# Optimization experiments

Measured on AMD Instinct MI355X. Metric: run time of the kernel, lower is better.

The kernel has to match this reference:

```python
import jax, jax.numpy as jnp
import numpy as np

N_EMBD = 1024
N_HEADS = 16
HEAD_SIZE = N_EMBD // N_HEADS
B, T = 1, 4096
LN_EPS = 1e-5


def setup_inputs() -> dict:
    key = jax.random.key(0)
    ks = jax.random.split(key, 12)
    s = lambda fan_in: 1.0 / np.sqrt(fan_in)
    return {
        "x": jax.random.normal(ks[0], (B, T, N_EMBD), dtype=jnp.float32),
        # per-head Q/K/V projections (no bias), stacked over heads: [H, C, hd]
        "Wq": jax.random.normal(ks[1], (N_HEADS, N_EMBD, HEAD_SIZE), dtype=jnp.float32) * s(N_EMBD),
        "Wk": jax.random.normal(ks[2], (N_HEADS, N_EMBD, HEAD_SIZE), dtype=jnp.float32) * s(N_EMBD),
        "Wv": jax.random.normal(ks[3], (N_HEADS, N_EMBD, HEAD_SIZE), dtype=jnp.float32) * s(N_EMBD),
        # output projection (with bias)
        "Wp": jax.random.normal(ks[4], (N_EMBD, N_EMBD), dtype=jnp.float32) * s(N_EMBD),
        "bp": jnp.zeros((N_EMBD,), dtype=jnp.float32),
        # FFN: Linear(C, 4C) -> ReLU -> Linear(4C, C)
        "W1": jax.random.normal(ks[5], (N_EMBD, 4 * N_EMBD), dtype=jnp.float32) * s(N_EMBD),
        "b1": jnp.zeros((4 * N_EMBD,), dtype=jnp.float32),
        "W2": jax.random.normal(ks[6], (4 * N_EMBD, N_EMBD), dtype=jnp.float32) * s(4 * N_EMBD),
        "b2": jnp.zeros((N_EMBD,), dtype=jnp.float32),
        # LayerNorms
        "g1": jnp.ones((N_EMBD,), dtype=jnp.float32),
        "be1": jnp.zeros((N_EMBD,), dtype=jnp.float32),
        "g2": jnp.ones((N_EMBD,), dtype=jnp.float32),
        "be2": jnp.zeros((N_EMBD,), dtype=jnp.float32),
    }


def _layernorm(x, gamma, beta):
    mu = jnp.mean(x, axis=-1, keepdims=True)
    var = jnp.mean(jnp.square(x - mu), axis=-1, keepdims=True)
    return (x - mu) * jax.lax.rsqrt(var + LN_EPS) * gamma + beta


def _block(x, Wq, Wk, Wv, Wp, bp, W1, b1, W2, b2, g1, be1, g2, be2):
    Bn, Tn, C = x.shape
    h = _layernorm(x, g1, be1)
    # per-head projections: [B, H, T, hd]
    q = jnp.einsum("btc,hcd->bhtd", h, Wq)
    k = jnp.einsum("btc,hcd->bhtd", h, Wk)
    v = jnp.einsum("btc,hcd->bhtd", h, Wv)
    # NOTE: original scales by C**-0.5 where C = n_embd (not head_size)
    scores = jnp.einsum("bhtd,bhsd->bhts", q, k) * (C ** -0.5)
    causal = jnp.tril(jnp.ones((Tn, Tn), dtype=bool))
    scores = jnp.where(causal, scores, -jnp.inf)
    w = jax.nn.softmax(scores, axis=-1)
    attn = jnp.einsum("bhts,bhsd->bhtd", w, v)
    # concat heads: [B, T, H*hd] = [B, T, C]
    attn = attn.transpose(0, 2, 1, 3).reshape(Bn, Tn, C)
    x = x + attn @ Wp + bp
    h2 = _layernorm(x, g2, be2)
    ff = jax.nn.relu(h2 @ W1 + b1) @ W2 + b2
    return x + ff


def reference(x, Wq, Wk, Wv, Wp, bp, W1, b1, W2, b2, g1, be1, g2, be2):
    return _block(x, Wq, Wk, Wv, Wp, bp, W1, b1, W2, b2, g1, be1, g2, be2)
```

## Files before the change

kernel.cpp:

```cpp
#include <hip/hip_runtime.h>
#include <cstdint>

typedef __attribute__((ext_vector_type(8))) short bf16x8;
typedef __attribute__((ext_vector_type(4))) float f32x4;
typedef __attribute__((ext_vector_type(16))) float f32x16;
typedef __attribute__((ext_vector_type(4))) unsigned int u32x4;

__device__ __forceinline__ short f2b(float f) {
  unsigned u = __builtin_bit_cast(unsigned, f);
  unsigned r = (u + 0x7fffu + ((u >> 16) & 1u)) >> 16;
  return (short)(unsigned short)r;
}
__device__ __forceinline__ float b2f(short s) {
  unsigned u = ((unsigned)(unsigned short)s) << 16;
  return __builtin_bit_cast(float, u);
}

__device__ __forceinline__ void gload16(void* lds_dst, const void* gsrc) {
  __builtin_amdgcn_global_load_lds(
      (const __attribute__((address_space(1))) void*)gsrc,
      (__attribute__((address_space(3))) void*)lds_dst, 16, 0, 0);
}

__device__ __forceinline__ unsigned cvtpk(float a, float b) {
  unsigned r;
  asm("v_cvt_pk_bf16_f32 %0, %1, %2" : "=v"(r) : "v"(a), "v"(b));
  return r;
}
__device__ __forceinline__ unsigned shflx32(unsigned v) {
  return (unsigned)__shfl_xor((int)v, 32);
}
__device__ __forceinline__ float exp2x(float x) {
  float r;
  asm("v_exp_f32 %0, %1" : "=v"(r) : "v"(x));
  return r;
}

__device__ __forceinline__ void plswap(unsigned &a, unsigned &b) {
#if __has_builtin(__builtin_amdgcn_permlane32_swap)
  auto r = __builtin_amdgcn_permlane32_swap((int)a, (int)b, false, false);
  a = (unsigned)r[0];
  b = (unsigned)r[1];
#else
  const bool lo = ((threadIdx.x & 63) < 32);
  unsigned ax = shflx32(a), bx = shflx32(b);
  unsigned na = lo ? a : bx;
  unsigned nb = lo ? ax : b;
  a = na; b = nb;
#endif
}

__global__ __launch_bounds__(256)
void prep_all(const float* __restrict__ Wq, const float* __restrict__ Wk,
              const float* __restrict__ Wv, const float* __restrict__ Wp,
              const float* __restrict__ W1, const float* __restrict__ W2,
              const float* __restrict__ x, const float* __restrict__ g1,
              const float* __restrict__ be1,
              short* __restrict__ WqkvT, short* __restrict__ WpT,
              short* __restrict__ W1T, short* __restrict__ W2T,
              short* __restrict__ hbuf)
{
  const int id = blockIdx.x;
  if (id < 12288) {
    __shared__ float tl[32][33];
    const int tx = threadIdx.x & 31;
    const int ty = threadIdx.x >> 5;
    if (id < 3072) {
      const int which = id >> 10;
      const int rem = id & 1023;
      const int head = rem >> 6;
      const int tile = rem & 63;
      const int tc = tile >> 1, td = tile & 1;
      const float* src = (which == 0 ? Wq : which == 1 ? Wk : Wv) + (long)head * 65536;
#pragma unroll
      for (int i2 = 0; i2 < 4; ++i2) {
        int i = ty + i2 * 8;
        tl[i][tx] = src[(long)(tc * 32 + i) * 64 + td * 32 + tx];
      }
      __syncthreads();
      const long base = (long)which * 1024 + head * 64 + td * 32;
#pragma unroll
      for (int i2 = 0; i2 < 4; ++i2) {
        int i = ty + i2 * 8;
        WqkvT[(base + i) * 1024 + tc * 32 + tx] = f2b(tl[tx][i]);
      }
    } else {
      const float* src;
      short* dst;
      int rows, cols, bx, by;
      if (id < 4096) {
        src = Wp; dst = WpT; rows = 1024; cols = 1024;
        const int k = id - 3072; bx = k & 31; by = k >> 5;
      } else if (id < 8192) {
        src = W1; dst = W1T; rows = 1024; cols = 4096;
        const int k = id - 4096; bx = k & 127; by = k >> 7;
      } else {
        src = W2; dst = W2T; rows = 4096; cols = 1024;
        const int k = id - 8192; bx = k & 31; by = k >> 5;
      }
#pragma unroll
      for (int i2 = 0; i2 < 4; ++i2) {
        int i = ty + i2 * 8;
        tl[i][tx] = src[(long)(by * 32 + i) * cols + bx * 32 + tx];
      }
      __syncthreads();
#pragma unroll
      for (int i2 = 0; i2 < 4; ++i2) {
        int i = ty + i2 * 8;
        dst[(long)(bx * 32 + i) * rows + by * 32 + tx] = f2b(tl[tx][i]);
      }
    }
  } else {
    const int row = id - 12288;
    const int t = threadIdx.x;
    const float4 v = ((const float4*)(x + (long)row * 1024))[t];
    float s = v.x + v.y + v.z + v.w;
    float ss = v.x * v.x + v.y * v.y + v.z * v.z + v.w * v.w;
#pragma unroll
    for (int off = 1; off < 64; off <<= 1) {
      s += __shfl_xor(s, off);
      ss += __shfl_xor(ss, off);
    }
    __shared__ float red[8];
    const int wave = t >> 6, lane = t & 63;
    if (lane == 0) { red[wave] = s; red[4 + wave] = ss; }
    __syncthreads();
    s = red[0] + red[1] + red[2] + red[3];
    ss = red[4] + red[5] + red[6] + red[7];
    const float mu = s * (1.f / 1024.f);
    const float rstd = rsqrtf(ss * (1.f / 1024.f) - mu * mu + 1e-5f);
    const float4 gv = ((const float4*)g1)[t];
    const float4 bv = ((const float4*)be1)[t];
    short4 ov;
    ov.x = f2b((v.x - mu) * rstd * gv.x + bv.x);
    ov.y = f2b((v.y - mu) * rstd * gv.y + bv.y);
    ov.z = f2b((v.z - mu) * rstd * gv.z + bv.z);
    ov.w = f2b((v.w - mu) * rstd * gv.w + bv.w);
    *(short4*)(hbuf + (long)row * 1024 + t * 4) = ov;
  }
}

__global__ void vtrans(const short* __restrict__ qkv, short* __restrict__ Vt)
{
  __shared__ short tl[32][33];
  const int t0 = blockIdx.x * 32;
  const int c0 = blockIdx.y * 32;
  const int head = c0 >> 6, d0 = c0 & 63;
  const int tx = threadIdx.x;
#pragma unroll
  for (int i2 = 0; i2 < 4; ++i2) {
    int i = threadIdx.y + i2 * 8;
    tl[i][tx] = qkv[(long)(t0 + i) * 3072 + 2048 + c0 + tx];
  }
  __syncthreads();
#pragma unroll
  for (int i2 = 0; i2 < 4; ++i2) {
    int i = threadIdx.y + i2 * 8;
    Vt[(long)head * 262144 + (long)(d0 + i) * 4096 + t0 + tx] = tl[tx][i];
  }
}

__global__ __launch_bounds__(256)
void layernorm_bf16(const float* __restrict__ x, const float* __restrict__ g,
                    const float* __restrict__ be, short* __restrict__ outp)
{
  const int row = blockIdx.x;
  const int t = threadIdx.x;
  const float4 v = ((const float4*)(x + (long)row * 1024))[t];
  float s = v.x + v.y + v.z + v.w;
  float ss = v.x * v.x + v.y * v.y + v.z * v.z + v.w * v.w;
#pragma unroll
  for (int off = 1; off < 64; off <<= 1) {
    s += __shfl_xor(s, off);
    ss += __shfl_xor(ss, off);
  }
  __shared__ float red[8];
  const int wave = t >> 6, lane = t & 63;
  if (lane == 0) { red[wave] = s; red[4 + wave] = ss; }
  __syncthreads();
  s = red[0] + red[1] + red[2] + red[3];
  ss = red[4] + red[5] + red[6] + red[7];
  const float mu = s * (1.f / 1024.f);
  const float rstd = rsqrtf(ss * (1.f / 1024.f) - mu * mu + 1e-5f);
  const float4 gv = ((const float4*)g)[t];
  const float4 bv = ((const float4*)be)[t];
  short4 ov;
  ov.x = f2b((v.x - mu) * rstd * gv.x + bv.x);
  ov.y = f2b((v.y - mu) * rstd * gv.y + bv.y);
  ov.z = f2b((v.z - mu) * rstd * gv.z + bv.z);
  ov.w = f2b((v.w - mu) * rstd * gv.w + bv.w);
  *(short4*)(outp + (long)row * 1024 + t * 4) = ov;
}

template<int EPI>
__global__ __launch_bounds__(512, 2)
void gemm128(const short* __restrict__ A, const short* __restrict__ Bt,
             int N, int K, int NT,
             short* __restrict__ Cb, float* __restrict__ Cf,
             const float* __restrict__ bias, const float* __restrict__ resid)
{
  __shared__ __align__(16) short As[2 * 8192];
  __shared__ __align__(16) short Bs[2 * 8192];
  const int tid = threadIdx.x;
  const int lane = tid & 63;
  const int wave = tid >> 6;
  const int wm = wave >> 2;
  const int wn = wave & 3;
  const int l15 = lane & 15, lg = lane >> 4;

  const int nwg = gridDim.x * gridDim.y;
  const int lin = blockIdx.y * gridDim.x + blockIdx.x;
  const int swz = (lin & 7) * (nwg >> 3) + (lin >> 3);
  const long m0 = (long)(swz / gridDim.x) * 128;
  const long n0 = (long)(swz % gridDim.x) * 128;

  const int rloc = lane >> 3;
  const int csrc = (lane & 7) ^ rloc;
  const short* Ag = A + (m0 + wave * 8 + rloc) * K + csrc * 8;
  const short* Bg = Bt + (n0 + wave * 8 + rloc) * K + csrc * 8;
  const int wbase = wave * 512;

  f32x4 acc[4][2] = {};

#define STAGE128(buf, kt)                                                     \
  do {                                                                        \
    gload16(As + (buf) * 8192 + wbase, Ag + (kt));                            \
    gload16(As + (buf) * 8192 + 4096 + wbase, Ag + (long)64 * K + (kt));      \
    gload16(Bs + (buf) * 8192 + wbase, Bg + (kt));                            \
    gload16(Bs + (buf) * 8192 + 4096 + wbase, Bg + (long)64 * K + (kt));      \
  } while (0)

  STAGE128(0, 0);
  STAGE128(1, 64);
  asm volatile("s_waitcnt vmcnt(4)" ::: "memory");
  __builtin_amdgcn_sched_barrier(0);
  __builtin_amdgcn_s_barrier();
  __builtin_amdgcn_sched_barrier(0);

  const int cA = l15 & 7;
  for (int t = 0; t < NT; ++t) {
    const char* Ab = (const char*)(As + (t & 1) * 8192);
    const char* Bb = (const char*)(Bs + (t & 1) * 8192);
#pragma unroll
    for (int kk = 0; kk < 2; ++kk) {
      bf16x8 af[4], bk[2];
#pragma unroll
      for (int mi = 0; mi < 4; ++mi)
        af[mi] = *(const bf16x8*)(Ab + (wm * 64 + mi * 16 + l15) * 128 + 16 * ((kk * 4 + lg) ^ cA));
#pragma unroll
      for (int ni = 0; ni < 2; ++ni)
        bk[ni] = *(const bf16x8*)(Bb + (wn * 32 + ni * 16 + l15) * 128 + 16 * ((kk * 4 + lg) ^ cA));
      __builtin_amdgcn_s_setprio(1);
#pragma unroll
      for (int mi = 0; mi < 4; ++mi)
#pragma unroll
        for (int ni = 0; ni < 2; ++ni)
          acc[mi][ni] = __builtin_amdgcn_mfma_f32_16x16x32_bf16(af[mi], bk[ni], acc[mi][ni], 0, 0, 0);
      __builtin_amdgcn_s_setprio(0);
    }
    if (t == NT - 1) break;
    __builtin_amdgcn_s_barrier();
    __builtin_amdgcn_sched_barrier(0);
    if (t + 2 < NT) {
      STAGE128(t & 1, (long)(t + 2) * 64);
      asm volatile("s_waitcnt vmcnt(4)" ::: "memory");
    } else {
      asm volatile("s_waitcnt vmcnt(0)" ::: "memory");
    }
    __builtin_amdgcn_sched_barrier(0);
    __builtin_amdgcn_s_barrier();
    __builtin_amdgcn_sched_barrier(0);
  }
#undef STAGE128

#pragma unroll
  for (int mi = 0; mi < 4; ++mi) {
#pragma unroll
    for (int ni = 0; ni < 2; ++ni) {
      const long col = n0 + wn * 32 + ni * 16 + l15;
#pragma unroll
      for (int r = 0; r < 4; ++r) {
        const long row = m0 + wm * 64 + mi * 16 + lg * 4 + r;
        const long idx = row * N + col;
        float v = acc[mi][ni][r];
        if (EPI == 0) {
          Cb[idx] = f2b(v);
        } else {
          Cf[idx] = v + bias[col] + resid[idx];
        }
      }
    }
  }
}

__device__ __forceinline__ void stage256(short* AsB, short* BsB,
                                         const short* Ag, const short* Bg,
                                         long kt, int K, int ldsoff)
{
#pragma unroll
  for (int p = 0; p < 4; ++p)
    gload16(AsB + p * 4096 + ldsoff, Ag + (long)p * 64 * K + kt);
#pragma unroll
  for (int p = 0; p < 4; ++p)
    gload16(BsB + p * 4096 + ldsoff, Bg + (long)p * 64 * K + kt);
}

template<int EPI>
__global__ __launch_bounds__(512, 2)
void gemm256(const short* __restrict__ A, const short* __restrict__ Bt,
             int N, int K, int NT,
             short* __restrict__ Cb, const float* __restrict__ bias)
{
  __shared__ __align__(16) short As[2 * 16384];
  __shared__ __align__(16) short Bs[2 * 16384];
  const int tid = threadIdx.x;
  const int lane = tid & 63;
  const int wave = tid >> 6;
  const int wm = wave >> 2;
  const int wn = wave & 3;
  const int l15 = lane & 15, lg = lane >> 4;

  const int nwg = gridDim.x * gridDim.y;
  const int lin = blockIdx.y * gridDim.x + blockIdx.x;
  const int swz = (lin & 7) * (nwg >> 3) + (lin >> 3);
  const long m0 = (long)(swz / gridDim.x) * 256;
  const long n0 = (long)(swz % gridDim.x) * 256;

  const int trow = tid >> 3;
  const int csrc = (tid & 7) ^ (trow & 7);
  const short* Ag = A + (m0 + trow) * K + csrc * 8;
  const short* Bg = Bt + (n0 + trow) * K + csrc * 8;
  const int ldsoff = wave * 512;

  f32x4 acc[8][4] = {};

  stage256(As, Bs, Ag, Bg, 0, K, ldsoff);
  asm volatile("s_waitcnt vmcnt(0)" ::: "memory");
  __builtin_amdgcn_sched_barrier(0);
  __builtin_amdgcn_s_barrier();
  __builtin_amdgcn_sched_barrier(0);

  const int cA = l15 & 7;
  for (int t = 0; t < NT; ++t) {
    const char* Ab = (const char*)(As + (t & 1) * 16384);
    const char* Bb = (const char*)(Bs + (t & 1) * 16384);
    short* Asn = As + ((t + 1) & 1) * 16384;
    short* Bsn = Bs + ((t + 1) & 1) * 16384;
    const bool more = (t + 1 < NT);
    const long ktn = (long)(t + 1) * 64;
    bf16x8 bk[4];
#pragma unroll
    for (int ph = 0; ph < 4; ++ph) {
      const int kk = ph >> 1;
      const int mh = (ph & 1) * 4;
      bf16x8 af[4];
#pragma unroll
      for (int mi = 0; mi < 4; ++mi)
        af[mi] = *(const bf16x8*)(Ab + (wm * 128 + (mh + mi) * 16 + l15) * 128 + 16 * ((kk * 4 + lg) ^ cA));
      if ((ph & 1) == 0) {
#pragma unroll
        for (int ni = 0; ni < 4; ++ni)
          bk[ni] = *(const bf16x8*)(Bb + (wn * 64 + ni * 16 + l15) * 128 + 16 * ((kk * 4 + lg) ^ cA));
      }
      if (more && ph == 0) {
#pragma unroll
        for (int p = 0; p < 4; ++p)
          gload16(Asn + p * 4096 + ldsoff, Ag + (long)p * 64 * K + ktn);
      }
      if (more && ph == 1) {
#pragma unroll
        for (int p = 0; p < 4; ++p)
          gload16(Bsn + p * 4096 + ldsoff, Bg + (long)p * 64 * K + ktn);
      }
      __builtin_amdgcn_s_barrier();
      asm volatile("s_waitcnt lgkmcnt(0)" ::: "memory");
      __builtin_amdgcn_sched_barrier(0);
      __builtin_amdgcn_s_setprio(1);
#pragma unroll
      for (int mi = 0; mi < 4; ++mi)
#pragma unroll
        for (int ni = 0; ni < 4; ++ni)
          acc[mh + mi][ni] = __builtin_amdgcn_mfma_f32_16x16x32_bf16(af[mi], bk[ni], acc[mh + mi][ni], 0, 0, 0);
      __builtin_amdgcn_s_setprio(0);
      if (ph == 3 && more) {
        asm volatile("s_waitcnt vmcnt(0)" ::: "memory");
        __builtin_amdgcn_sched_barrier(0);
      }
      __builtin_amdgcn_s_barrier();
      __builtin_amdgcn_sched_barrier(0);
    }
  }

#pragma unroll
  for (int mi = 0; mi < 8; ++mi) {
#pragma unroll
    for (int ni = 0; ni < 4; ++ni) {
      const long col = n0 + wn * 64 + ni * 16 + l15;
      const float bb = (EPI == 2) ? bias[col] : 0.f;
#pragma unroll
      for (int r = 0; r < 4; ++r) {
        const long row = m0 + wm * 128 + mi * 16 + lg * 4 + r;
        float v = acc[mi][ni][r];
        if (EPI == 2) { v += bb; v = v > 0.f ? v : 0.f; }
        Cb[row * N + col] = f2b(v);
      }
    }
  }
}

__device__ __forceinline__ void stage_k32(short* lds, const short* gRowBase)
{
  const int lane = threadIdx.x & 63;
  const int rloc = lane >> 3;
  const int cs = (lane & 7) ^ rloc;
#pragma unroll
  for (int p = 0; p < 4; ++p)
    gload16(lds + p * 512, gRowBase + (long)(p * 8 + rloc) * 3072 + cs * 8);
}
__device__ __forceinline__ void stage_v32(short* lds, const short* vHeadBase, int t0)
{
  const int lane = threadIdx.x & 63;
  const int rloc = lane >> 3;
  const int cs = (lane & 7) ^ rloc;
#pragma unroll
  for (int p = 0; p < 4; ++p) {
    const int row = p * 8 + rloc;
    const int d = row + ((cs & 4) << 3);
    gload16(lds + p * 512, vHeadBase + (long)d * 4096 + t0 + (cs & 3) * 8);
  }
}

__global__ __launch_bounds__(256)
void attn_fwd6(const short* __restrict__ qkv, const short* __restrict__ Vt,
               short* __restrict__ outp)
{
  __shared__ __align__(16) short POOL[4 * 4096];
  __shared__ float lAll[64];
  short* const OB = POOL;

  const int tid = threadIdx.x;
  const int lane = tid & 63;
  const int wave = tid >> 6;
  const int wq = wave & 1;
  const int ks = wave >> 1;
  const int l31 = lane & 31;
  const int h = lane >> 5;
  const int rs = l31 & 7;

  const int id = blockIdx.x;
  const int head = ((id & 7) << 1) | (id >> 8);
  const int bx = (id >> 3) & 31;

  const short* Qg = qkv + head * 64;
  const short* Kg = qkv + 1024 + head * 64;
  const short* Vg = Vt + (long)head * 262144;

  short* Kw = POOL + wave * 4096;

  bf16x8 onesf;
#pragma unroll
  for (int j = 0; j < 8; ++j) onesf[j] = (short)0x3F80;

  for (int ph = 0; ph < 2; ++ph) {
    const int qsuper = ph ? (63 - bx) : bx;
    const int q0 = qsuper * 64 + wq * 32;
    const int q = q0 + l31;
    const int nt = qsuper + 1;

    bf16x8 qf[4];
#pragma unroll
    for (int d = 0; d < 4; ++d) {
      bf16x8 tq = *(const bf16x8*)(Qg + (long)q * 3072 + d * 16 + h * 8);
#pragma unroll
      for (int j = 0; j < 8; ++j) tq[j] = f2b(b2f(tq[j]) * (0.03125f * 1.44269504f));
      qf[d] = tq;
    }

    f32x16 o0 = {}, o1 = {}, lacc = {};

    stage_k32(Kw, Kg + (long)(ks * 32) * 3072);
    stage_v32(Kw + 2048, Vg, ks * 32);

    for (int t = 0; t < nt; ++t) {
      asm volatile("s_waitcnt vmcnt(0)" ::: "memory");
      __builtin_amdgcn_sched_barrier(0);
      const char* Kb = (const char*)Kw;
      const char* Vb = Kb + 4096;
      const bf16x8 kf0 = *(const bf16x8*)(Kb + l31 * 128 + 16 * ((0 + h) ^ rs));
      const bf16x8 kf1 = *(const bf16x8*)(Kb + l31 * 128 + 16 * ((2 + h) ^ rs));
      const bf16x8 kf2 = *(const bf16x8*)(Kb + l31 * 128 + 16 * ((4 + h) ^ rs));
      const bf16x8 kf3 = *(const bf16x8*)(Kb + l31 * 128 + 16 * ((6 + h) ^ rs));
      const bf16x8 vf00 = *(const bf16x8*)(Vb + l31 * 128 + 16 * ((0 + h) ^ rs));
      const bf16x8 vf01 = *(const bf16x8*)(Vb + l31 * 128 + 16 * ((2 + h) ^ rs));
      const bf16x8 vf10 = *(const bf16x8*)(Vb + l31 * 128 + 16 * ((4 + h) ^ rs));
      const bf16x8 vf11 = *(const bf16x8*)(Vb + l31 * 128 + 16 * ((6 + h) ^ rs));
      asm volatile("s_waitcnt lgkmcnt(0)" ::: "memory");
      __builtin_amdgcn_sched_barrier(0);
      if (t + 1 < nt) {
        stage_k32(Kw, Kg + (long)((t + 1) * 64 + ks * 32) * 3072);
        stage_v32(Kw + 2048, Vg, (t + 1) * 64 + ks * 32);
      }
      f32x16 s = {};
      __builtin_amdgcn_s_setprio(1);
      s = __builtin_amdgcn_mfma_f32_32x32x16_bf16(kf0, qf[0], s, 0, 0, 0);
      s = __builtin_amdgcn_mfma_f32_32x32x16_bf16(kf1, qf[1], s, 0, 0, 0);
      s = __builtin_amdgcn_mfma_f32_32x32x16_bf16(kf2, qf[2], s, 0, 0, 0);
      s = __builtin_amdgcn_mfma_f32_32x32x16_bf16(kf3, qf[3], s, 0, 0, 0);
      __builtin_amdgcn_s_setprio(0);
      if (t == qsuper) {
        const int kb0 = t * 64 + ks * 32 + 4 * h;
#pragma unroll
        for (int r = 0; r < 16; ++r) {
          const int k0 = kb0 + (r & 3) + 8 * (r >> 2);
          if (k0 > q) s[r] = -INFINITY;
        }
      }
#pragma unroll
      for (int r = 0; r < 16; ++r) s[r] = exp2x(s[r]);
      unsigned P0 = cvtpk(s[0], s[1]),   P1 = cvtpk(s[2], s[3]);
      unsigned P2 = cvtpk(s[4], s[5]),   P3 = cvtpk(s[6], s[7]);
      unsigned P4 = cvtpk(s[8], s[9]),   P5 = cvtpk(s[10], s[11]);
      unsigned P6 = cvtpk(s[12], s[13]), P7 = cvtpk(s[14], s[15]);
      plswap(P0, P2); plswap(P1, P3); plswap(P4, P6); plswap(P5, P7);
      u32x4 f0, f1;
      f0[0] = P0; f0[1] = P1; f0[2] = P2; f0[3] = P3;
      f1[0] = P4; f1[1] = P5; f1[2] = P6; f1[3] = P7;
      const bf16x8 pa0 = __builtin_bit_cast(bf16x8, f0);
      const bf16x8 pa1 = __builtin_bit_cast(bf16x8, f1);
      __builtin_amdgcn_s_setprio(1);
      o0 = __builtin_amdgcn_mfma_f32_32x32x16_bf16(pa0, vf00, o0, 0, 0, 0);
      o0 = __builtin_amdgcn_mfma_f32_32x32x16_bf16(pa1, vf01, o0, 0, 0, 0);
      o1 = __builtin_amdgcn_mfma_f32_32x32x16_bf16(pa0, vf10, o1, 0, 0, 0);
      o1 = __builtin_amdgcn_mfma_f32_32x32x16_bf16(pa1, vf11, o1, 0, 0, 0);
      lacc = __builtin_amdgcn_mfma_f32_32x32x16_bf16(pa0, onesf, lacc, 0, 0, 0);
      lacc = __builtin_amdgcn_mfma_f32_32x32x16_bf16(pa1, onesf, lacc, 0, 0, 0);
      __builtin_amdgcn_s_setprio(0);
    }

    __syncthreads();
    if (ks == 1) {
#pragma unroll
      for (int r = 0; r < 16; ++r) {
        const int qq = wq * 32 + (r & 3) + 8 * (r >> 2) + 4 * h;
        OB[qq * 64 + l31] = f2b(o0[r]);
        OB[qq * 64 + 32 + l31] = f2b(o1[r]);
      }
      if (l31 == 0) {
#pragma unroll
        for (int r = 0; r < 16; ++r) {
          const int qq = wq * 32 + (r & 3) + 8 * (r >> 2) + 4 * h;
          lAll[qq] = lacc[r];
        }
      }
    }
    __syncthreads();
    if (ks == 0) {
#pragma unroll
      for (int r = 0; r < 16; ++r) {
        const int qq = wq * 32 + (r & 3) + 8 * (r >> 2) + 4 * h;
        const float inv = 1.f / (lacc[r] + lAll[qq]);
        const long qr = (long)qsuper * 64 + qq;
        const float v0 = o0[r] + b2f(OB[qq * 64 + l31]);
        const float v1 = o1[r] + b2f(OB[qq * 64 + 32 + l31]);
        outp[qr * 1024 + head * 64 + l31] = f2b(v0 * inv);
        outp[qr * 1024 + head * 64 + 32 + l31] = f2b(v1 * inv);
      }
    }
    __syncthreads();
  }
}

extern "C" void kernel_launch(void* const* d_in, const int* in_sizes, int n_in,
                              void* d_out, int out_size, void* d_ws, size_t ws_size,
                              hipStream_t stream)
{
  (void)in_sizes; (void)n_in; (void)out_size; (void)ws_size;
  const float* x   = (const float*)d_in[0];
  const float* Wq  = (const float*)d_in[1];
  const float* Wk  = (const float*)d_in[2];
  const float* Wv  = (const float*)d_in[3];
  const float* Wp  = (const float*)d_in[4];
  const float* bp  = (const float*)d_in[5];
  const float* W1  = (const float*)d_in[6];
  const float* b1  = (const float*)d_in[7];
  const float* W2  = (const float*)d_in[8];
  const float* b2  = (const float*)d_in[9];
  const float* g1  = (const float*)d_in[10];
  const float* be1 = (const float*)d_in[11];
  const float* g2  = (const float*)d_in[12];
  const float* be2 = (const float*)d_in[13];
  float* out = (float*)d_out;

  char* ws = (char*)d_ws;
  const size_t MB = 1ull << 20;
  short* WqkvT = (short*)(ws + 0 * MB);
  short* WpT   = (short*)(ws + 6 * MB);
  short* W1T   = (short*)(ws + 8 * MB);
  short* W2T   = (short*)(ws + 16 * MB);
  short* hbuf  = (short*)(ws + 24 * MB);
  short* qkvb  = (short*)(ws + 32 * MB);
  short* attnb = (short*)(ws + 56 * MB);
  float* x1    = (float*)(ws + 64 * MB);
  short* Vtb   = (short*)(ws + 64 * MB);

  prep_all<<<16384, 256, 0, stream>>>(Wq, Wk, Wv, Wp, W1, W2, x, g1, be1,
                                      WqkvT, WpT, W1T, W2T, hbuf);
  gemm256<0><<<dim3(12, 16), 512, 0, stream>>>(hbuf, WqkvT, 3072, 1024, 16,
                                               qkvb, nullptr);
  vtrans<<<dim3(128, 32), dim3(32, 8), 0, stream>>>(qkvb, Vtb);
  attn_fwd6<<<512, 256, 0, stream>>>(qkvb, Vtb, attnb);
  gemm128<1><<<dim3(8, 32), 512, 0, stream>>>(attnb, WpT, 1024, 1024, 16,
                                              nullptr, x1, bp, x);
  layernorm_bf16<<<4096, 256, 0, stream>>>(x1, g2, be2, hbuf);
  gemm256<2><<<dim3(16, 16), 512, 0, stream>>>(hbuf, W1T, 4096, 1024, 16,
                                               qkvb, b1);
  gemm128<1><<<dim3(8, 32), 512, 0, stream>>>(qkvb, W2T, 1024, 4096, 64,
                                              nullptr, out, b2, x1);
}
```

Baseline: 246.8 us.

## Split-K the output-projection and FFN2 GEMMs and fuse the reduction with LayerNorm

The two N=1024 GEMMs (attention output projection and FFN down-projection) now run as split-K over two halves. This doubles the grid from 256 to 512 workgroups to fill the CUs better. Each half writes bf16 partials, and a separate reduction kernel sums them with the bias and residual. For the projection, that reduction is fused with the second LayerNorm, replacing the standalone layernorm kernel. The trade-off is extra partial-buffer traffic, reduced precision from storing partials in bf16, and reuse of workspace regions (the weight buffers WqkvT/W1T) as partial storage.

```diff
diff --git a/kernel.cpp b/kernel.cpp
--- a/kernel.cpp
+++ b/kernel.cpp
@@ -160,13 +160,142 @@
   }
 }
 
+__global__ __launch_bounds__(512, 2)
+void gemm128sk(const short* __restrict__ A, const short* __restrict__ Bt,
+               int N, int K, int NT,
+               short* __restrict__ p0, short* __restrict__ p1)
+{
+  __shared__ __align__(16) short As[2 * 8192];
+  __shared__ __align__(16) short Bs[2 * 8192];
+  const int tid = threadIdx.x;
+  const int lane = tid & 63;
+  const int wave = tid >> 6;
+  const int wm = wave >> 2;
+  const int wn = wave & 3;
+  const int l15 = lane & 15, lg = lane >> 4;
+
+  const int nwg = gridDim.x * gridDim.y;
+  const int lin = blockIdx.y * gridDim.x + blockIdx.x;
+  const int swz = (lin & 7) * (nwg >> 3) + (lin >> 3);
+  const int my = swz >> 3;
+  const int half = my >> 5;
+  const long m0 = (long)(my & 31) * 128;
+  const long n0 = (long)(swz & 7) * 128;
+  const long k0 = (long)half * (K >> 1);
+  short* const Cb = half ? p1 : p0;
+
+  const int rloc = lane >> 3;
+  const int csrc = (lane & 7) ^ rloc;
+  const short* Ag = A + (m0 + wave * 8 + rloc) * K + csrc * 8 + k0;
+  const short* Bg = Bt + (n0 + wave * 8 + rloc) * K + csrc * 8 + k0;
+  const int wbase = wave * 512;
+
+  f32x4 acc[4][2] = {};
+
+#define STAGESK(buf, kt)                                                      \
+  do {                                                                        \
+    gload16(As + (buf) * 8192 + wbase, Ag + (kt));                            \
+    gload16(As + (buf) * 8192 + 4096 + wbase, Ag + (long)64 * K + (kt));      \
+    gload16(Bs + (buf) * 8192 + wbase, Bg + (kt));                            \
+    gload16(Bs + (buf) * 8192 + 4096 + wbase, Bg + (long)64 * K + (kt));      \
+  } while (0)
+
+  STAGESK(0, 0);
+  STAGESK(1, 64);
+  asm volatile("s_waitcnt vmcnt(4)" ::: "memory");
+  __builtin_amdgcn_sched_barrier(0);
+  __builtin_amdgcn_s_barrier();
+  __builtin_amdgcn_sched_barrier(0);
+
+  const int cA = l15 & 7;
+  for (int t = 0; t < NT; ++t) {
+    const char* Ab = (const char*)(As + (t & 1) * 8192);
+    const char* Bb = (const char*)(Bs + (t & 1) * 8192);
+#pragma unroll
+    for (int kk = 0; kk < 2; ++kk) {
+      bf16x8 af[4], bk[2];
+#pragma unroll
+      for (int mi = 0; mi < 4; ++mi)
+        af[mi] = *(const bf16x8*)(Ab + (wm * 64 + mi * 16 + l15) * 128 + 16 * ((kk * 4 + lg) ^ cA));
+#pragma unroll
+      for (int ni = 0; ni < 2; ++ni)
+        bk[ni] = *(const bf16x8*)(Bb + (wn * 32 + ni * 16 + l15) * 128 + 16 * ((kk * 4 + lg) ^ cA));
+      __builtin_amdgcn_s_setprio(1);
+#pragma unroll
+      for (int mi = 0; mi < 4; ++mi)
+#pragma unroll
+        for (int ni = 0; ni < 2; ++ni)
+          acc[mi][ni] = __builtin_amdgcn_mfma_f32_16x16x32_bf16(af[mi], bk[ni], acc[mi][ni], 0, 0, 0);
+      __builtin_amdgcn_s_setprio(0);
+    }
+    if (t == NT - 1) break;
+    __builtin_amdgcn_s_barrier();
+    __builtin_amdgcn_sched_barrier(0);
+    if (t + 2 < NT) {
+      STAGESK(t & 1, (long)(t + 2) * 64);
+      asm volatile("s_waitcnt vmcnt(4)" ::: "memory");
+    } else {
+      asm volatile("s_waitcnt vmcnt(0)" ::: "memory");
+    }
+    __builtin_amdgcn_sched_barrier(0);
+    __builtin_amdgcn_s_barrier();
+    __builtin_amdgcn_sched_barrier(0);
+  }
+#undef STAGESK
+
+#pragma unroll
+  for (int mi = 0; mi < 4; ++mi) {
+#pragma unroll
+    for (int ni = 0; ni < 2; ++ni) {
+      const long col = n0 + wn * 32 + ni * 16 + l15;
+#pragma unroll
+      for (int r = 0; r < 4; ++r) {
+        const long row = m0 + wm * 64 + mi * 16 + lg * 4 + r;
+        Cb[row * N + col] = f2b(acc[mi][ni][r]);
+      }
+    }
+  }
+}
+
 __global__ __launch_bounds__(256)
-void layernorm_bf16(const float* __restrict__ x, const float* __restrict__ g,
-                    const float* __restrict__ be, short* __restrict__ outp)
-{
-  const int row = blockIdx.x;
+void reduce_ffn2(const short* __restrict__ p0, const short* __restrict__ p1,
+                 const float* __restrict__ bias, const float* __restrict__ resid,
+                 float* __restrict__ outp)
+{
+  const long row = blockIdx.x;
   const int t = threadIdx.x;
-  const float4 v = ((const float4*)(x + (long)row * 1024))[t];
+  const long base = row * 1024 + t * 4;
+  const short4 a = *(const short4*)(p0 + base);
+  const short4 b = *(const short4*)(p1 + base);
+  const float4 rv = *(const float4*)(resid + base);
+  const float4 bv = ((const float4*)bias)[t];
+  float4 o;
+  o.x = b2f(a.x) + b2f(b.x) + bv.x + rv.x;
+  o.y = b2f(a.y) + b2f(b.y) + bv.y + rv.y;
+  o.z = b2f(a.z) + b2f(b.z) + bv.z + rv.z;
+  o.w = b2f(a.w) + b2f(b.w) + bv.w + rv.w;
+  *(float4*)(outp + base) = o;
+}
+
+__global__ __launch_bounds__(256)
+void reduce_ln2(const short* __restrict__ p0, const short* __restrict__ p1,
+                const float* __restrict__ bp, const float* __restrict__ xres,
+                const float* __restrict__ g2, const float* __restrict__ be2,
+                float* __restrict__ x1, short* __restrict__ hbuf)
+{
+  const long row = blockIdx.x;
+  const int t = threadIdx.x;
+  const long base = row * 1024 + t * 4;
+  const short4 a = *(const short4*)(p0 + base);
+  const short4 b = *(const short4*)(p1 + base);
+  const float4 rv = *(const float4*)(xres + base);
+  const float4 bpv = ((const float4*)bp)[t];
+  float4 v;
+  v.x = b2f(a.x) + b2f(b.x) + bpv.x + rv.x;
+  v.y = b2f(a.y) + b2f(b.y) + bpv.y + rv.y;
+  v.z = b2f(a.z) + b2f(b.z) + bpv.z + rv.z;
+  v.w = b2f(a.w) + b2f(b.w) + bpv.w + rv.w;
+  *(float4*)(x1 + base) = v;
   float s = v.x + v.y + v.z + v.w;
   float ss = v.x * v.x + v.y * v.y + v.z * v.z + v.w * v.w;
 #pragma unroll
@@ -182,115 +311,14 @@
   ss = red[4] + red[5] + red[6] + red[7];
   const float mu = s * (1.f / 1024.f);
   const float rstd = rsqrtf(ss * (1.f / 1024.f) - mu * mu + 1e-5f);
-  const float4 gv = ((const float4*)g)[t];
-  const float4 bv = ((const float4*)be)[t];
+  const float4 gv = ((const float4*)g2)[t];
+  const float4 bv = ((const float4*)be2)[t];
   short4 ov;
   ov.x = f2b((v.x - mu) * rstd * gv.x + bv.x);
   ov.y = f2b((v.y - mu) * rstd * gv.y + bv.y);
   ov.z = f2b((v.z - mu) * rstd * gv.z + bv.z);
   ov.w = f2b((v.w - mu) * rstd * gv.w + bv.w);
-  *(short4*)(outp + (long)row * 1024 + t * 4) = ov;
-}
-
-template<int EPI>
-__global__ __launch_bounds__(512, 2)
-void gemm128(const short* __restrict__ A, const short* __restrict__ Bt,
-             int N, int K, int NT,
-             short* __restrict__ Cb, float* __restrict__ Cf,
-             const float* __restrict__ bias, const float* __restrict__ resid)
-{
-  __shared__ __align__(16) short As[2 * 8192];
-  __shared__ __align__(16) short Bs[2 * 8192];
-  const int tid = threadIdx.x;
-  const int lane = tid & 63;
-  const int wave = tid >> 6;
-  const int wm = wave >> 2;
-  const int wn = wave & 3;
-  const int l15 = lane & 15, lg = lane >> 4;
-
-  const int nwg = gridDim.x * gridDim.y;
-  const int lin = blockIdx.y * gridDim.x + blockIdx.x;
-  const int swz = (lin & 7) * (nwg >> 3) + (lin >> 3);
-  const long m0 = (long)(swz / gridDim.x) * 128;
-  const long n0 = (long)(swz % gridDim.x) * 128;
-
-  const int rloc = lane >> 3;
-  const int csrc = (lane & 7) ^ rloc;
-  const short* Ag = A + (m0 + wave * 8 + rloc) * K + csrc * 8;
-  const short* Bg = Bt + (n0 + wave * 8 + rloc) * K + csrc * 8;
-  const int wbase = wave * 512;
-
-  f32x4 acc[4][2] = {};
-
-#define STAGE128(buf, kt)                                                     \
-  do {                                                                        \
-    gload16(As + (buf) * 8192 + wbase, Ag + (kt));                            \
-    gload16(As + (buf) * 8192 + 4096 + wbase, Ag + (long)64 * K + (kt));      \
-    gload16(Bs + (buf) * 8192 + wbase, Bg + (kt));                            \
-    gload16(Bs + (buf) * 8192 + 4096 + wbase, Bg + (long)64 * K + (kt));      \
-  } while (0)
-
-  STAGE128(0, 0);
-  STAGE128(1, 64);
-  asm volatile("s_waitcnt vmcnt(4)" ::: "memory");
-  __builtin_amdgcn_sched_barrier(0);
-  __builtin_amdgcn_s_barrier();
-  __builtin_amdgcn_sched_barrier(0);
-
-  const int cA = l15 & 7;
-  for (int t = 0; t < NT; ++t) {
-    const char* Ab = (const char*)(As + (t & 1) * 8192);
-    const char* Bb = (const char*)(Bs + (t & 1) * 8192);
-#pragma unroll
-    for (int kk = 0; kk < 2; ++kk) {
-      bf16x8 af[4], bk[2];
-#pragma unroll
-      for (int mi = 0; mi < 4; ++mi)
-        af[mi] = *(const bf16x8*)(Ab + (wm * 64 + mi * 16 + l15) * 128 + 16 * ((kk * 4 + lg) ^ cA));
-#pragma unroll
-      for (int ni = 0; ni < 2; ++ni)
-        bk[ni] = *(const bf16x8*)(Bb + (wn * 32 + ni * 16 + l15) * 128 + 16 * ((kk * 4 + lg) ^ cA));
-      __builtin_amdgcn_s_setprio(1);
-#pragma unroll
-      for (int mi = 0; mi < 4; ++mi)
-#pragma unroll
-        for (int ni = 0; ni < 2; ++ni)
-          acc[mi][ni] = __builtin_amdgcn_mfma_f32_16x16x32_bf16(af[mi], bk[ni], acc[mi][ni], 0, 0, 0);
-      __builtin_amdgcn_s_setprio(0);
-    }
-    if (t == NT - 1) break;
-    __builtin_amdgcn_s_barrier();
-    __builtin_amdgcn_sched_barrier(0);
-    if (t + 2 < NT) {
-      STAGE128(t & 1, (long)(t + 2) * 64);
-      asm volatile("s_waitcnt vmcnt(4)" ::: "memory");
-    } else {
-      asm volatile("s_waitcnt vmcnt(0)" ::: "memory");
-    }
-    __builtin_amdgcn_sched_barrier(0);
-    __builtin_amdgcn_s_barrier();
-    __builtin_amdgcn_sched_barrier(0);
-  }
-#undef STAGE128
-
-#pragma unroll
-  for (int mi = 0; mi < 4; ++mi) {
-#pragma unroll
-    for (int ni = 0; ni < 2; ++ni) {
-      const long col = n0 + wn * 32 + ni * 16 + l15;
-#pragma unroll
-      for (int r = 0; r < 4; ++r) {
-        const long row = m0 + wm * 64 + mi * 16 + lg * 4 + r;
-        const long idx = row * N + col;
-        float v = acc[mi][ni][r];
-        if (EPI == 0) {
-          Cb[idx] = f2b(v);
-        } else {
-          Cf[idx] = v + bias[col] + resid[idx];
-        }
-      }
-    }
-  }
+  *(short4*)(hbuf + base) = ov;
 }
 
 __device__ __forceinline__ void stage256(short* AsB, short* BsB,
@@ -602,6 +630,10 @@
   short* attnb = (short*)(ws + 56 * MB);
   float* x1    = (float*)(ws + 64 * MB);
   short* Vtb   = (short*)(ws + 64 * MB);
+  short* p0p   = (short*)(ws + 32 * MB);
+  short* p1p   = (short*)(ws + 40 * MB);
+  short* p0buf = (short*)(ws + 0 * MB);
+  short* p1buf = (short*)(ws + 8 * MB);
 
   prep_all<<<16384, 256, 0, stream>>>(Wq, Wk, Wv, Wp, W1, W2, x, g1, be1,
                                       WqkvT, WpT, W1T, W2T, hbuf);
@@ -609,11 +641,12 @@
                                                qkvb, nullptr);
   vtrans<<<dim3(128, 32), dim3(32, 8), 0, stream>>>(qkvb, Vtb);
   attn_fwd6<<<512, 256, 0, stream>>>(qkvb, Vtb, attnb);
-  gemm128<1><<<dim3(8, 32), 512, 0, stream>>>(attnb, WpT, 1024, 1024, 16,
-                                              nullptr, x1, bp, x);
-  layernorm_bf16<<<4096, 256, 0, stream>>>(x1, g2, be2, hbuf);
+  gemm128sk<<<dim3(8, 64), 512, 0, stream>>>(attnb, WpT, 1024, 1024, 8,
+                                             p0p, p1p);
+  reduce_ln2<<<4096, 256, 0, stream>>>(p0p, p1p, bp, x, g2, be2, x1, hbuf);
   gemm256<2><<<dim3(16, 16), 512, 0, stream>>>(hbuf, W1T, 4096, 1024, 16,
                                                qkvb, b1);
-  gemm128<1><<<dim3(8, 32), 512, 0, stream>>>(qkvb, W2T, 1024, 4096, 64,
-                                              nullptr, out, b2, x1);
-}
+  gemm128sk<<<dim3(8, 64), 512, 0, stream>>>(qkvb, W2T, 1024, 4096, 32,
+                                             p0buf, p1buf);
+  reduce_ffn2<<<4096, 256, 0, stream>>>(p0buf, p1buf, b2, x1, out);
+}
```

Result: faster. 230.2 us, median of 2 (-6.8%).
